# Performance work log

Measured on AMD Instinct MI355X. Metric: run time of the kernel, lower is better.

Reference implementation:

```python
import jax, jax.numpy as jnp
import numpy as np

B, S, N, D = 2, 2048, 16, 64


def setup_inputs() -> dict:
    key = jax.random.key(0)
    kq, kk, kv = jax.random.split(key, 3)
    query = jax.random.normal(kq, (B, S, N, D), dtype=jnp.float32)
    key_t = jax.random.normal(kk, (B, S, N, D), dtype=jnp.float32)
    value = jax.random.normal(kv, (B, S, N, D), dtype=jnp.float32)
    mask = jnp.ones((B, 1, S, S), dtype=jnp.int32)
    return {"query": query, "key": key_t, "value": value, "mask": mask}


def reference(query, key, value, mask):
    d_k = query.shape[-1]
    # [b, n, q, k] attention scores
    scores = jnp.einsum('bqnd,bknd->bnqk', query, key) / jnp.sqrt(jnp.float32(d_k))
    scores = jnp.where(mask == 0, -jnp.inf, scores)
    # NOTE: faithful to the source, softmax is over dim=1 (the HEAD axis),
    # not the key axis. Dropout prob is 0.0 -> identity.
    attn_weights = jax.nn.softmax(scores, axis=1)
    out = jnp.einsum('bnqk,bknd->bnqd', attn_weights, value)
    return out
```

## Files before the change

### kernel.cpp

```cpp
#include <hip/hip_runtime.h>
#include <hip/hip_bf16.h>


#define B_ 2
#define S_ 2048
#define N_ 16
#define D_ 64
#define TQ 32
#define TK 32
#define NT 64

typedef __bf16 bf16x4 __attribute__((ext_vector_type(4)));
typedef __bf16 bf16x8 __attribute__((ext_vector_type(8)));
typedef float  f32x16 __attribute__((ext_vector_type(16)));
typedef unsigned int uint32x4 __attribute__((ext_vector_type(4)));

#define QSCALE 0.18033688011112042f

static __device__ __forceinline__ unsigned int cvt_pk_bf16(float a, float b) {
    unsigned int r;
    asm("v_cvt_pk_bf16_f32 %0, %1, %2" : "=v"(r) : "v"(a), "v"(b));
    return r;
}
static __device__ __forceinline__ void permlane_swap(unsigned int& a, unsigned int& b) {
    asm("v_permlane32_swap_b32 %0, %1" : "+v"(a), "+v"(b));
}

__global__ __launch_bounds__(256) void cvt_qk_pack_kernel(
    const float* __restrict__ Qf, const float* __restrict__ Kf,
    __bf16* __restrict__ QP, __bf16* __restrict__ KP)
{
    const int z = blockIdx.z;
    const float* src = (z < B_) ? Qf : Kf;
    __bf16*      dst = (z < B_) ? QP : KP;
    const float scale = (z < B_) ? QSCALE : 1.0f;
    const int b  = (z < B_) ? z : z - B_;
    const int n  = blockIdx.y;
    const int st = blockIdx.x;
    const int t  = threadIdx.x;
    const int ks   = t >> 6;
    const int lane = t & 63;
    const int lo   = lane & 31;
    const int hi   = lane >> 5;

    const float* p = &src[(((size_t)b * S_ + st * 32 + lo) * N_ + n) * D_ + ks * 16 + hi * 8];
    const float4 a0 = *(const float4*)p;
    const float4 a1 = *(const float4*)(p + 4);
    bf16x8 o;
    o[0] = (__bf16)(a0.x * scale); o[1] = (__bf16)(a0.y * scale);
    o[2] = (__bf16)(a0.z * scale); o[3] = (__bf16)(a0.w * scale);
    o[4] = (__bf16)(a1.x * scale); o[5] = (__bf16)(a1.y * scale);
    o[6] = (__bf16)(a1.z * scale); o[7] = (__bf16)(a1.w * scale);
    *(bf16x8*)&dst[(((size_t)b * N_ + n) * NT + st) * 2048 + (size_t)t * 8] = o;
}

__global__ __launch_bounds__(256) void cvt_v_pack_kernel(
    const float* __restrict__ V, __bf16* __restrict__ VP)
{
    __shared__ __bf16 tile[64][68];
    const int s0 = blockIdx.x * 64;
    const int n  = blockIdx.y;
    const int b  = blockIdx.z;
    const int t  = threadIdx.x;

    {
        const int d4 = (t & 15) * 4;
        const int sr = t >> 4;
        #pragma unroll
        for (int r = 0; r < 4; ++r) {
            const int s = sr + r * 16;
            const float4 v = *(const float4*)&V[(((size_t)b * S_ + s0 + s) * N_ + n) * D_ + d4];
            tile[s][d4 + 0] = (__bf16)v.x;
            tile[s][d4 + 1] = (__bf16)v.y;
            tile[s][d4 + 2] = (__bf16)v.z;
            tile[s][d4 + 3] = (__bf16)v.w;
        }
    }
    __syncthreads();
    {
        const int kstep = t >> 7;
        const int dt    = (t >> 6) & 1;
        const int lane  = t & 63;
        const int lo    = lane & 31;
        const int hi    = lane >> 5;
        #pragma unroll
        for (int kt_sub = 0; kt_sub < 2; ++kt_sub) {
            bf16x8 o;
            #pragma unroll
            for (int j = 0; j < 8; ++j)
                o[j] = tile[kt_sub * 32 + kstep * 16 + hi * 8 + j][dt * 32 + lo];
            const size_t kt = (size_t)(blockIdx.x * 2 + kt_sub);
            *(bf16x8*)&VP[(((size_t)b * N_ + n) * NT + kt) * 2048 + (size_t)t * 8] = o;
        }
    }
}

__global__ __launch_bounds__(256, 3) void pass1_z_kernel(
    const __bf16* __restrict__ QP, const __bf16* __restrict__ KP,
    const int* __restrict__ M, float* __restrict__ Zrt)
{
    const int tid  = threadIdx.x;
    const int wv   = tid >> 6;
    const int lane = tid & 63;
    const int lo   = lane & 31;
    const int hi   = lane >> 5;

    const int ktA = (blockIdx.x * 4 + wv) * 2;
    const int qt  = blockIdx.y;
    const int b   = blockIdx.z;
    const int k0A = ktA * TK;
    const int q0  = qt * TQ;

    const __bf16* Qp = QP + ((size_t)b * N_ * NT + qt) * 2048 + (size_t)lane * 8;
    const __bf16* Kp = KP + ((size_t)b * N_ * NT + ktA) * 2048 + (size_t)lane * 8;

    f32x16 zA = {}, zB = {};
    #pragma unroll 2
    for (int h = 0; h < N_; ++h) {
        const __bf16* Qh = Qp + (size_t)h * NT * 2048;
        const __bf16* Kh = Kp + (size_t)h * NT * 2048;
        bf16x8 qf[4], ka[4], kb[4];
        #pragma unroll
        for (int ks = 0; ks < 4; ++ks) {
            qf[ks] = *(const bf16x8*)(Qh + ks * 512);
            ka[ks] = *(const bf16x8*)(Kh + ks * 512);
            kb[ks] = *(const bf16x8*)(Kh + 2048 + ks * 512);
        }
        f32x16 sA = {}, sB = {};
        #pragma unroll
        for (int ks = 0; ks < 4; ++ks)
            sA = __builtin_amdgcn_mfma_f32_32x32x16_bf16(ka[ks], qf[ks], sA, 0, 0, 0);
        #pragma unroll
        for (int ks = 0; ks < 4; ++ks)
            sB = __builtin_amdgcn_mfma_f32_32x32x16_bf16(kb[ks], qf[ks], sB, 0, 0, 0);
        #pragma unroll
        for (int r = 0; r < 16; ++r) {
            zA[r] += __builtin_amdgcn_exp2f(sA[r]);
            zB[r] += __builtin_amdgcn_exp2f(sB[r]);
        }
    }

    const size_t mb = (size_t)b * S_ * S_;
    int ok = 1;
    #pragma unroll
    for (int r = 0; r < 16; ++r) {
        const int2 mm = *(const int2*)&M[mb + (size_t)(q0 + 2 * r + hi) * S_ + k0A + 2 * lo];
        ok &= (mm.x != 0) & (mm.y != 0);
    }

    float vA[16], vB[16];
    #pragma unroll
    for (int r = 0; r < 16; ++r) {
        vA[r] = __builtin_amdgcn_rcpf(zA[r]);
        vB[r] = __builtin_amdgcn_rcpf(zB[r]);
    }

    if (!__all(ok)) {
        #pragma unroll
        for (int r = 0; r < 16; ++r) {
            const int kap = (r & 3) + 8 * (r >> 2) + 4 * hi;
            const size_t rowb = mb + (size_t)(q0 + lo) * S_ + k0A;
            if (M[rowb + kap] == 0)      vA[r] = __builtin_nanf("");
            if (M[rowb + 32 + kap] == 0) vB[r] = __builtin_nanf("");
        }
    }

    float* ZA = Zrt + (((size_t)b * NT + ktA) * NT + qt) * 1024 + (size_t)lane * 4;
    float* ZB = ZA + (size_t)NT * 1024;
    #pragma unroll
    for (int c = 0; c < 4; ++c) {
        *(float4*)(ZA + c * 256) = make_float4(vA[4*c], vA[4*c+1], vA[4*c+2], vA[4*c+3]);
        *(float4*)(ZB + c * 256) = make_float4(vB[4*c], vB[4*c+1], vB[4*c+2], vB[4*c+3]);
    }
}

__global__ __launch_bounds__(256, 4) void pass2_av_kernel(
    const __bf16* __restrict__ QP, const __bf16* __restrict__ KP,
    const __bf16* __restrict__ VP, const float* __restrict__ Zrt,
    float* __restrict__ O)
{
    __shared__ __align__(16) float obuf[4][16 * D_];

    const int tid  = threadIdx.x;
    const int wv   = tid >> 6;
    const int lane = tid & 63;
    const int lo   = lane & 31;
    const int hi   = lane >> 5;

    const int qt = blockIdx.x;
    const int n  = blockIdx.y;
    const int b  = blockIdx.z;
    const int q0 = qt * TQ;

    const __bf16* Qh = QP + (((size_t)b * N_ + n) * NT + qt) * 2048 + (size_t)lane * 8;
    const __bf16* Kh = KP + (((size_t)b * N_ + n) * NT) * 2048 + (size_t)lane * 8;
    const __bf16* Vh = VP + (((size_t)b * N_ + n) * NT) * 2048 + (size_t)lane * 8;
    const float*  Zh = Zrt + (size_t)b * NT * NT * 1024 + (size_t)lane * 4;

    bf16x8 qf[4];
    #pragma unroll
    for (int ks = 0; ks < 4; ++ks)
        qf[ks] = *(const bf16x8*)(Qh + ks * 512);

    f32x16 o0 = {};
    f32x16 o1 = {};

    #pragma unroll 2
    for (int t = 0; t < 16; ++t) {
        const int kt = wv * 16 + t;
        const __bf16* Kt = Kh + (size_t)kt * 2048;
        const __bf16* Vt = Vh + (size_t)kt * 2048;
        const float*  Zt = Zh + ((size_t)kt * NT + qt) * 1024;

        float4 z0 = *(const float4*)(Zt);
        float4 z1 = *(const float4*)(Zt + 256);
        float4 z2 = *(const float4*)(Zt + 512);
        float4 z3 = *(const float4*)(Zt + 768);
        float zr[16] = { z0.x, z0.y, z0.z, z0.w,  z1.x, z1.y, z1.z, z1.w,
                         z2.x, z2.y, z2.z, z2.w,  z3.x, z3.y, z3.z, z3.w };

        bf16x8 vf[2][2];
        #pragma unroll
        for (int kstep = 0; kstep < 2; ++kstep)
            #pragma unroll
            for (int dt = 0; dt < 2; ++dt)
                vf[kstep][dt] = *(const bf16x8*)(Vt + (kstep * 2 + dt) * 512);

        f32x16 s = {};
        #pragma unroll
        for (int ks = 0; ks < 4; ++ks) {
            bf16x8 kf = *(const bf16x8*)(Kt + ks * 512);
            s = __builtin_amdgcn_mfma_f32_32x32x16_bf16(kf, qf[ks], s, 0, 0, 0);
        }

        float w[16];
        #pragma unroll
        for (int r = 0; r < 16; ++r) w[r] = __builtin_amdgcn_exp2f(s[r]) * zr[r];

        #pragma unroll
        for (int kstep = 0; kstep < 2; ++kstep) {
            const int e = kstep * 8;
            unsigned int d0 = cvt_pk_bf16(w[e + 0], w[e + 1]);
            unsigned int d1 = cvt_pk_bf16(w[e + 2], w[e + 3]);
            unsigned int d2 = cvt_pk_bf16(w[e + 4], w[e + 5]);
            unsigned int d3 = cvt_pk_bf16(w[e + 6], w[e + 7]);
            permlane_swap(d0, d2);
            permlane_swap(d1, d3);
            uint32x4 u; u[0] = d0; u[1] = d1; u[2] = d2; u[3] = d3;
            const bf16x8 pa = __builtin_bit_cast(bf16x8, u);
            o0 = __builtin_amdgcn_mfma_f32_32x32x16_bf16(pa, vf[kstep][0], o0, 0, 0, 0);
            o1 = __builtin_amdgcn_mfma_f32_32x32x16_bf16(pa, vf[kstep][1], o1, 0, 0, 0);
        }
    }

    #pragma unroll
    for (int half = 0; half < 2; ++half) {
        if (half) __syncthreads();
        #pragma unroll
        for (int r8 = 0; r8 < 8; ++r8) {
            const int r  = half * 8 + r8;
            const int lr = (r8 & 3) + 8 * (r8 >> 2) + 4 * hi;
            obuf[wv][lr * D_ + lo]      = o0[r];
            obuf[wv][lr * D_ + 32 + lo] = o1[r];
        }
        __syncthreads();
        const int e0 = tid * 4;
        float a0 = 0.f, a1 = 0.f, a2 = 0.f, a3 = 0.f;
        #pragma unroll
        for (int w = 0; w < 4; ++w) {
            const float4 x = *(const float4*)&obuf[w][e0];
            a0 += x.x; a1 += x.y; a2 += x.z; a3 += x.w;
        }
        const int q = half * 16 + (e0 >> 6);
        const int d = e0 & 63;
        *(float4*)&O[(((size_t)b * N_ + n) * S_ + q0 + q) * (size_t)D_ + d]
            = make_float4(a0, a1, a2, a3);
    }
}

__global__ __launch_bounds__(1024) void sdpa_headsm_kernel(
    const float* __restrict__ Q, const float* __restrict__ K,
    const float* __restrict__ V, const int* __restrict__ M,
    float* __restrict__ O)
{
    __shared__ __align__(16) __bf16 pbuf[N_][TQ][40];

    const int tid  = threadIdx.x;
    const int n    = tid >> 6;
    const int lane = tid & 63;
    const int lo   = lane & 31;
    const int hi   = lane >> 5;

    const int q0 = blockIdx.x * TQ;
    const int b  = blockIdx.y;
    const int kz = blockIdx.z;
    const int FITERS = S_ / TK / 4;

    bf16x8 qf[4];
    {
        const float* qrow = Q + (((size_t)b * S_ + (size_t)(q0 + lo)) * N_ + n) * D_;
        #pragma unroll
        for (int ks = 0; ks < 4; ++ks) {
            const float* p = qrow + ks * 16 + hi * 8;
            float4 a0 = *(const float4*)(p);
            float4 a1 = *(const float4*)(p + 4);
            bf16x8 f;
            f[0] = (__bf16)a0.x; f[1] = (__bf16)a0.y;
            f[2] = (__bf16)a0.z; f[3] = (__bf16)a0.w;
            f[4] = (__bf16)a1.x; f[5] = (__bf16)a1.y;
            f[6] = (__bf16)a1.z; f[7] = (__bf16)a1.w;
            qf[ks] = f;
        }
    }

    f32x16 o0 = {};
    f32x16 o1 = {};

    for (int it = 0; it < FITERS; ++it) {
        const int k0 = (kz * FITERS + it) * TK;

        f32x16 s = {};
        #pragma unroll
        for (int ks = 0; ks < 4; ++ks) {
            const float* krow = K + (((size_t)b * S_ + (size_t)(k0 + lo)) * N_ + n) * D_
                                  + ks * 16 + hi * 8;
            float4 a0 = *(const float4*)(krow);
            float4 a1 = *(const float4*)(krow + 4);
            bf16x8 f;
            f[0] = (__bf16)a0.x; f[1] = (__bf16)a0.y;
            f[2] = (__bf16)a0.z; f[3] = (__bf16)a0.w;
            f[4] = (__bf16)a1.x; f[5] = (__bf16)a1.y;
            f[6] = (__bf16)a1.z; f[7] = (__bf16)a1.w;
            s = __builtin_amdgcn_mfma_f32_32x32x16_bf16(qf[ks], f, s, 0, 0, 0);
        }

        bf16x8 vf[2][2];
        #pragma unroll
        for (int kstep = 0; kstep < 2; ++kstep) {
            #pragma unroll
            for (int dt = 0; dt < 2; ++dt) {
                bf16x8 f;
                #pragma unroll
                for (int j = 0; j < 8; ++j) {
                    const int key = k0 + kstep * 16 + hi * 8 + j;
                    f[j] = (__bf16)V[(((size_t)b * S_ + key) * N_ + n) * D_ + dt * 32 + lo];
                }
                vf[kstep][dt] = f;
            }
        }

        #pragma unroll
        for (int r = 0; r < 16; ++r) {
            const int row = (r & 3) + 8 * (r >> 2) + 4 * hi;
            pbuf[n][row][lo] = (__bf16)__builtin_amdgcn_exp2f(s[r] * QSCALE);
        }

        __syncthreads();

        {
            const int tq = tid >> 5;
            const int tk = tid & 31;
            const int m = M[(size_t)b * S_ * S_ + (size_t)(q0 + tq) * S_ + (k0 + tk)];
            float pv[16];
            float sum = 0.f;
            #pragma unroll
            for (int j = 0; j < 16; ++j) { pv[j] = (float)pbuf[j][tq][tk]; sum += pv[j]; }
            const float rd = m ? (1.0f / sum) : __builtin_nanf("");
            #pragma unroll
            for (int j = 0; j < 16; ++j) pbuf[j][tq][tk] = (__bf16)(pv[j] * rd);
        }

        __syncthreads();

        #pragma unroll
        for (int kstep = 0; kstep < 2; ++kstep) {
            bf16x8 wf = *(const bf16x8*)&pbuf[n][lo][kstep * 16 + hi * 8];
            o0 = __builtin_amdgcn_mfma_f32_32x32x16_bf16(wf, vf[kstep][0], o0, 0, 0, 0);
            o1 = __builtin_amdgcn_mfma_f32_32x32x16_bf16(wf, vf[kstep][1], o1, 0, 0, 0);
        }

        __syncthreads();
    }

    #pragma unroll
    for (int r = 0; r < 16; ++r) {
        const int row = (r & 3) + 8 * (r >> 2) + 4 * hi;
        const size_t base = (((size_t)b * N_ + n) * S_ + (q0 + row)) * (size_t)D_;
        atomicAdd(&O[base + lo],      o0[r]);
        atomicAdd(&O[base + 32 + lo], o1[r]);
    }
}

extern "C" void kernel_launch(void* const* d_in, const int* in_sizes, int n_in,
                              void* d_out, int out_size, void* d_ws, size_t ws_size,
                              hipStream_t stream) {
    const float* Q = (const float*)d_in[0];
    const float* K = (const float*)d_in[1];
    const float* V = (const float*)d_in[2];
    const int*   M = (const int*)d_in[3];
    float* O = (float*)d_out;

    const size_t per  = (size_t)B_ * N_ * NT * 2048;
    const size_t zcnt = (size_t)B_ * NT * NT * 1024;
    const size_t need = 3 * per * sizeof(__bf16) + zcnt * sizeof(float);

    if (ws_size >= need) {
        __bf16* QP = (__bf16*)d_ws;
        __bf16* KP = QP + per;
        __bf16* VP = KP + per;
        float*  Zrt = (float*)(VP + per);
        cvt_qk_pack_kernel<<<dim3(NT, N_, B_ * 2), dim3(256), 0, stream>>>(Q, K, QP, KP);
        cvt_v_pack_kernel<<<dim3(S_ / 64, N_, B_), dim3(256), 0, stream>>>(V, VP);
        pass1_z_kernel<<<dim3(NT / 8, NT, B_), dim3(256), 0, stream>>>(QP, KP, M, Zrt);
        pass2_av_kernel<<<dim3(NT, N_, B_), dim3(256), 0, stream>>>(QP, KP, VP, Zrt, O);
    } else {
        hipMemsetAsync(d_out, 0, (size_t)out_size * sizeof(float), stream);
        sdpa_headsm_kernel<<<dim3(S_ / TQ, B_, 4), dim3(1024), 0, stream>>>(Q, K, V, M, O);
    }
}
```

Baseline: 220.4 us.

## Process two query tiles per wave and store head-softmax reciprocals as bf16

Both passes now handle two 32-row query tiles per block, so each loaded K/V fragment is reused for two tiles and the grid shrinks by half. The per-(q,k) reciprocal normalizer buffer is stored as bf16 instead of fp32, halving its write and read traffic between the two passes. The mask check now reads int4 rows to cover the larger tile, and occupancy hints drop to 2 blocks per CU. In exchange, register pressure goes up, there are fewer blocks to fill the GPU, and the normalizer loses precision, which adds error to the output.

Result: slower. 239.0 us (+8.4%).

```diff
diff --git a/kernel.cpp b/kernel.cpp
--- a/kernel.cpp
+++ b/kernel.cpp
@@ -95,9 +95,9 @@
     }
 }
 
-__global__ __launch_bounds__(256, 3) void pass1_z_kernel(
+__global__ __launch_bounds__(256, 2) void pass1_z_kernel(
     const __bf16* __restrict__ QP, const __bf16* __restrict__ KP,
-    const int* __restrict__ M, float* __restrict__ Zrt)
+    const int* __restrict__ M, __bf16* __restrict__ Zrb)
 {
     const int tid  = threadIdx.x;
     const int wv   = tid >> 6;
@@ -106,80 +106,103 @@
     const int hi   = lane >> 5;
 
     const int ktA = (blockIdx.x * 4 + wv) * 2;
-    const int qt  = blockIdx.y;
+    const int qt0 = blockIdx.y * 2;
     const int b   = blockIdx.z;
     const int k0A = ktA * TK;
-    const int q0  = qt * TQ;
-
-    const __bf16* Qp = QP + ((size_t)b * N_ * NT + qt) * 2048 + (size_t)lane * 8;
+    const int q0  = qt0 * TQ;
+
+    const __bf16* Qp = QP + ((size_t)b * N_ * NT + qt0) * 2048 + (size_t)lane * 8;
     const __bf16* Kp = KP + ((size_t)b * N_ * NT + ktA) * 2048 + (size_t)lane * 8;
 
-    f32x16 zA = {}, zB = {};
-    #pragma unroll 2
+    f32x16 zAA = {}, zAB = {}, zBA = {}, zBB = {};
     for (int h = 0; h < N_; ++h) {
         const __bf16* Qh = Qp + (size_t)h * NT * 2048;
         const __bf16* Kh = Kp + (size_t)h * NT * 2048;
-        bf16x8 qf[4], ka[4], kb[4];
+        bf16x8 q0f[4], q1f[4], ka[4], kb[4];
         #pragma unroll
         for (int ks = 0; ks < 4; ++ks) {
-            qf[ks] = *(const bf16x8*)(Qh + ks * 512);
-            ka[ks] = *(const bf16x8*)(Kh + ks * 512);
-            kb[ks] = *(const bf16x8*)(Kh + 2048 + ks * 512);
-        }
-        f32x16 sA = {}, sB = {};
-        #pragma unroll
-        for (int ks = 0; ks < 4; ++ks)
-            sA = __builtin_amdgcn_mfma_f32_32x32x16_bf16(ka[ks], qf[ks], sA, 0, 0, 0);
-        #pragma unroll
-        for (int ks = 0; ks < 4; ++ks)
-            sB = __builtin_amdgcn_mfma_f32_32x32x16_bf16(kb[ks], qf[ks], sB, 0, 0, 0);
-        #pragma unroll
-        for (int r = 0; r < 16; ++r) {
-            zA[r] += __builtin_amdgcn_exp2f(sA[r]);
-            zB[r] += __builtin_amdgcn_exp2f(sB[r]);
-        }
+            q0f[ks] = *(const bf16x8*)(Qh + ks * 512);
+            q1f[ks] = *(const bf16x8*)(Qh + 2048 + ks * 512);
+            ka[ks]  = *(const bf16x8*)(Kh + ks * 512);
+            kb[ks]  = *(const bf16x8*)(Kh + 2048 + ks * 512);
+        }
+        f32x16 s;
+        s = (f32x16){};
+        #pragma unroll
+        for (int ks = 0; ks < 4; ++ks) s = __builtin_amdgcn_mfma_f32_32x32x16_bf16(ka[ks], q0f[ks], s, 0, 0, 0);
+        #pragma unroll
+        for (int r = 0; r < 16; ++r) zAA[r] += __builtin_amdgcn_exp2f(s[r]);
+        s = (f32x16){};
+        #pragma unroll
+        for (int ks = 0; ks < 4; ++ks) s = __builtin_amdgcn_mfma_f32_32x32x16_bf16(ka[ks], q1f[ks], s, 0, 0, 0);
+        #pragma unroll
+        for (int r = 0; r < 16; ++r) zAB[r] += __builtin_amdgcn_exp2f(s[r]);
+        s = (f32x16){};
+        #pragma unroll
+        for (int ks = 0; ks < 4; ++ks) s = __builtin_amdgcn_mfma_f32_32x32x16_bf16(kb[ks], q0f[ks], s, 0, 0, 0);
+        #pragma unroll
+        for (int r = 0; r < 16; ++r) zBA[r] += __builtin_amdgcn_exp2f(s[r]);
+        s = (f32x16){};
+        #pragma unroll
+        for (int ks = 0; ks < 4; ++ks) s = __builtin_amdgcn_mfma_f32_32x32x16_bf16(kb[ks], q1f[ks], s, 0, 0, 0);
+        #pragma unroll
+        for (int r = 0; r < 16; ++r) zBB[r] += __builtin_amdgcn_exp2f(s[r]);
     }
 
     const size_t mb = (size_t)b * S_ * S_;
     int ok = 1;
     #pragma unroll
     for (int r = 0; r < 16; ++r) {
-        const int2 mm = *(const int2*)&M[mb + (size_t)(q0 + 2 * r + hi) * S_ + k0A + 2 * lo];
-        ok &= (mm.x != 0) & (mm.y != 0);
-    }
-
-    float vA[16], vB[16];
+        const int4 mm = *(const int4*)&M[mb + (size_t)(q0 + 4 * r + (lane >> 4)) * S_
+                                         + k0A + (lane & 15) * 4];
+        ok &= (mm.x != 0) & (mm.y != 0) & (mm.z != 0) & (mm.w != 0);
+    }
+
+    float vAA[16], vAB[16], vBA[16], vBB[16];
     #pragma unroll
     for (int r = 0; r < 16; ++r) {
-        vA[r] = __builtin_amdgcn_rcpf(zA[r]);
-        vB[r] = __builtin_amdgcn_rcpf(zB[r]);
+        vAA[r] = __builtin_amdgcn_rcpf(zAA[r]);
+        vAB[r] = __builtin_amdgcn_rcpf(zAB[r]);
+        vBA[r] = __builtin_amdgcn_rcpf(zBA[r]);
+        vBB[r] = __builtin_amdgcn_rcpf(zBB[r]);
     }
 
     if (!__all(ok)) {
         #pragma unroll
         for (int r = 0; r < 16; ++r) {
             const int kap = (r & 3) + 8 * (r >> 2) + 4 * hi;
-            const size_t rowb = mb + (size_t)(q0 + lo) * S_ + k0A;
-            if (M[rowb + kap] == 0)      vA[r] = __builtin_nanf("");
-            if (M[rowb + 32 + kap] == 0) vB[r] = __builtin_nanf("");
-        }
-    }
-
-    float* ZA = Zrt + (((size_t)b * NT + ktA) * NT + qt) * 1024 + (size_t)lane * 4;
-    float* ZB = ZA + (size_t)NT * 1024;
-    #pragma unroll
-    for (int c = 0; c < 4; ++c) {
-        *(float4*)(ZA + c * 256) = make_float4(vA[4*c], vA[4*c+1], vA[4*c+2], vA[4*c+3]);
-        *(float4*)(ZB + c * 256) = make_float4(vB[4*c], vB[4*c+1], vB[4*c+2], vB[4*c+3]);
-    }
-}
-
-__global__ __launch_bounds__(256, 4) void pass2_av_kernel(
+            const size_t rowA = mb + (size_t)(q0 + lo) * S_;
+            const size_t rowB = mb + (size_t)(q0 + 32 + lo) * S_;
+            if (M[rowA + k0A + kap] == 0)      vAA[r] = __builtin_nanf("");
+            if (M[rowB + k0A + kap] == 0)      vAB[r] = __builtin_nanf("");
+            if (M[rowA + k0A + 32 + kap] == 0) vBA[r] = __builtin_nanf("");
+            if (M[rowB + k0A + 32 + kap] == 0) vBB[r] = __builtin_nanf("");
+        }
+    }
+
+    auto store_tile = [&](const float (&v)[16], int kt_, int qt_) {
+        __bf16* Zt = Zrb + (((size_t)b * NT + kt_) * NT + qt_) * 1024 + (size_t)lane * 8;
+        #pragma unroll
+        for (int g = 0; g < 2; ++g) {
+            uint32x4 u;
+            #pragma unroll
+            for (int i = 0; i < 4; ++i)
+                u[i] = cvt_pk_bf16(v[g * 8 + 2 * i], v[g * 8 + 2 * i + 1]);
+            *(bf16x8*)(Zt + g * 512) = __builtin_bit_cast(bf16x8, u);
+        }
+    };
+    store_tile(vAA, ktA,     qt0);
+    store_tile(vAB, ktA,     qt0 + 1);
+    store_tile(vBA, ktA + 1, qt0);
+    store_tile(vBB, ktA + 1, qt0 + 1);
+}
+
+__global__ __launch_bounds__(256, 2) void pass2_av_kernel(
     const __bf16* __restrict__ QP, const __bf16* __restrict__ KP,
-    const __bf16* __restrict__ VP, const float* __restrict__ Zrt,
+    const __bf16* __restrict__ VP, const __bf16* __restrict__ Zrb,
     float* __restrict__ O)
 {
-    __shared__ __align__(16) float obuf[4][16 * D_];
+    __shared__ __align__(16) float obuf[4][TQ * D_];
 
     const int tid  = threadIdx.x;
     const int wv   = tid >> 6;
@@ -187,38 +210,39 @@
     const int lo   = lane & 31;
     const int hi   = lane >> 5;
 
-    const int qt = blockIdx.x;
-    const int n  = blockIdx.y;
-    const int b  = blockIdx.z;
-    const int q0 = qt * TQ;
-
-    const __bf16* Qh = QP + (((size_t)b * N_ + n) * NT + qt) * 2048 + (size_t)lane * 8;
+    const int n   = blockIdx.x;
+    const int qt0 = blockIdx.y * 2;
+    const int b   = blockIdx.z;
+
+    const __bf16* Qh = QP + (((size_t)b * N_ + n) * NT + qt0) * 2048 + (size_t)lane * 8;
     const __bf16* Kh = KP + (((size_t)b * N_ + n) * NT) * 2048 + (size_t)lane * 8;
     const __bf16* Vh = VP + (((size_t)b * N_ + n) * NT) * 2048 + (size_t)lane * 8;
-    const float*  Zh = Zrt + (size_t)b * NT * NT * 1024 + (size_t)lane * 4;
-
-    bf16x8 qf[4];
+    const __bf16* Zb = Zrb + (size_t)b * NT * NT * 1024 + (size_t)lane * 8;
+
+    bf16x8 qf0[4], qf1[4];
     #pragma unroll
-    for (int ks = 0; ks < 4; ++ks)
-        qf[ks] = *(const bf16x8*)(Qh + ks * 512);
-
-    f32x16 o0 = {};
-    f32x16 o1 = {};
-
-    #pragma unroll 2
+    for (int ks = 0; ks < 4; ++ks) {
+        qf0[ks] = *(const bf16x8*)(Qh + ks * 512);
+        qf1[ks] = *(const bf16x8*)(Qh + 2048 + ks * 512);
+    }
+
+    f32x16 o00 = {}, o01 = {};
+    f32x16 o10 = {}, o11 = {};
+
     for (int t = 0; t < 16; ++t) {
         const int kt = wv * 16 + t;
         const __bf16* Kt = Kh + (size_t)kt * 2048;
         const __bf16* Vt = Vh + (size_t)kt * 2048;
-        const float*  Zt = Zh + ((size_t)kt * NT + qt) * 1024;
-
-        float4 z0 = *(const float4*)(Zt);
-        float4 z1 = *(const float4*)(Zt + 256);
-        float4 z2 = *(const float4*)(Zt + 512);
-        float4 z3 = *(const float4*)(Zt + 768);
-        float zr[16] = { z0.x, z0.y, z0.z, z0.w,  z1.x, z1.y, z1.z, z1.w,
-                         z2.x, z2.y, z2.z, z2.w,  z3.x, z3.y, z3.z, z3.w };
-
+        const __bf16* Zt = Zb + ((size_t)kt * NT + qt0) * 1024;
+
+        const bf16x8 z0a = *(const bf16x8*)(Zt);
+        const bf16x8 z0b = *(const bf16x8*)(Zt + 512);
+        const bf16x8 z1a = *(const bf16x8*)(Zt + 1024);
+        const bf16x8 z1b = *(const bf16x8*)(Zt + 1536);
+
+        bf16x8 kf[4];
+        #pragma unroll
+        for (int ks = 0; ks < 4; ++ks) kf[ks] = *(const bf16x8*)(Kt + ks * 512);
         bf16x8 vf[2][2];
         #pragma unroll
         for (int kstep = 0; kstep < 2; ++kstep)
@@ -226,56 +250,84 @@
             for (int dt = 0; dt < 2; ++dt)
                 vf[kstep][dt] = *(const bf16x8*)(Vt + (kstep * 2 + dt) * 512);
 
-        f32x16 s = {};
+        f32x16 s0 = {}, s1 = {};
         #pragma unroll
         for (int ks = 0; ks < 4; ++ks) {
-            bf16x8 kf = *(const bf16x8*)(Kt + ks * 512);
-            s = __builtin_amdgcn_mfma_f32_32x32x16_bf16(kf, qf[ks], s, 0, 0, 0);
-        }
-
-        float w[16];
-        #pragma unroll
-        for (int r = 0; r < 16; ++r) w[r] = __builtin_amdgcn_exp2f(s[r]) * zr[r];
-
-        #pragma unroll
-        for (int kstep = 0; kstep < 2; ++kstep) {
-            const int e = kstep * 8;
-            unsigned int d0 = cvt_pk_bf16(w[e + 0], w[e + 1]);
-            unsigned int d1 = cvt_pk_bf16(w[e + 2], w[e + 3]);
-            unsigned int d2 = cvt_pk_bf16(w[e + 4], w[e + 5]);
-            unsigned int d3 = cvt_pk_bf16(w[e + 6], w[e + 7]);
-            permlane_swap(d0, d2);
-            permlane_swap(d1, d3);
-            uint32x4 u; u[0] = d0; u[1] = d1; u[2] = d2; u[3] = d3;
-            const bf16x8 pa = __builtin_bit_cast(bf16x8, u);
-            o0 = __builtin_amdgcn_mfma_f32_32x32x16_bf16(pa, vf[kstep][0], o0, 0, 0, 0);
-            o1 = __builtin_amdgcn_mfma_f32_32x32x16_bf16(pa, vf[kstep][1], o1, 0, 0, 0);
-        }
-    }
-
-    #pragma unroll
-    for (int half = 0; half < 2; ++half) {
-        if (half) __syncthreads();
-        #pragma unroll
-        for (int r8 = 0; r8 < 8; ++r8) {
-            const int r  = half * 8 + r8;
-            const int lr = (r8 & 3) + 8 * (r8 >> 2) + 4 * hi;
-            obuf[wv][lr * D_ + lo]      = o0[r];
-            obuf[wv][lr * D_ + 32 + lo] = o1[r];
+            s0 = __builtin_amdgcn_mfma_f32_32x32x16_bf16(kf[ks], qf0[ks], s0, 0, 0, 0);
+            s1 = __builtin_amdgcn_mfma_f32_32x32x16_bf16(kf[ks], qf1[ks], s1, 0, 0, 0);
+        }
+
+        {
+            float w[16];
+            #pragma unroll
+            for (int r = 0; r < 8; ++r)  w[r] = __builtin_amdgcn_exp2f(s0[r]) * (float)z0a[r];
+            #pragma unroll
+            for (int r = 8; r < 16; ++r) w[r] = __builtin_amdgcn_exp2f(s0[r]) * (float)z0b[r - 8];
+            #pragma unroll
+            for (int kstep = 0; kstep < 2; ++kstep) {
+                const int e = kstep * 8;
+                unsigned int d0 = cvt_pk_bf16(w[e + 0], w[e + 1]);
+                unsigned int d1 = cvt_pk_bf16(w[e + 2], w[e + 3]);
+                unsigned int d2 = cvt_pk_bf16(w[e + 4], w[e + 5]);
+                unsigned int d3 = cvt_pk_bf16(w[e + 6], w[e + 7]);
+                permlane_swap(d0, d2);
+                permlane_swap(d1, d3);
+                uint32x4 u; u[0] = d0; u[1] = d1; u[2] = d2; u[3] = d3;
+                const bf16x8 pa = __builtin_bit_cast(bf16x8, u);
+                o00 = __builtin_amdgcn_mfma_f32_32x32x16_bf16(pa, vf[kstep][0], o00, 0, 0, 0);
+                o01 = __builtin_amdgcn_mfma_f32_32x32x16_bf16(pa, vf[kstep][1], o01, 0, 0, 0);
+            }
+        }
+        {
+            float w[16];
+            #pragma unroll
+            for (int r = 0; r < 8; ++r)  w[r] = __builtin_amdgcn_exp2f(s1[r]) * (float)z1a[r];
+            #pragma unroll
+            for (int r = 8; r < 16; ++r) w[r] = __builtin_amdgcn_exp2f(s1[r]) * (float)z1b[r - 8];
+            #pragma unroll
+            for (int kstep = 0; kstep < 2; ++kstep) {
+                const int e = kstep * 8;
+                unsigned int d0 = cvt_pk_bf16(w[e + 0], w[e + 1]);
+                unsigned int d1 = cvt_pk_bf16(w[e + 2], w[e + 3]);
+                unsigned int d2 = cvt_pk_bf16(w[e + 4], w[e + 5]);
+                unsigned int d3 = cvt_pk_bf16(w[e + 6], w[e + 7]);
+                permlane_swap(d0, d2);
+                permlane_swap(d1, d3);
+                uint32x4 u; u[0] = d0; u[1] = d1; u[2] = d2; u[3] = d3;
+                const bf16x8 pa = __builtin_bit_cast(bf16x8, u);
+                o10 = __builtin_amdgcn_mfma_f32_32x32x16_bf16(pa, vf[kstep][0], o10, 0, 0, 0);
+                o11 = __builtin_amdgcn_mfma_f32_32x32x16_bf16(pa, vf[kstep][1], o11, 0, 0, 0);
+            }
+        }
+    }
+
+    auto combine_store = [&](const f32x16& a0, const f32x16& a1, int qt_) {
+        #pragma unroll
+        for (int r = 0; r < 16; ++r) {
+            const int row = (r & 3) + 8 * (r >> 2) + 4 * hi;
+            obuf[wv][row * D_ + lo]      = a0[r];
+            obuf[wv][row * D_ + 32 + lo] = a1[r];
         }
         __syncthreads();
-        const int e0 = tid * 4;
-        float a0 = 0.f, a1 = 0.f, a2 = 0.f, a3 = 0.f;
+        const int e0 = tid * 8;
+        float b0 = 0.f, b1 = 0.f, b2 = 0.f, b3 = 0.f;
+        float b4 = 0.f, b5 = 0.f, b6 = 0.f, b7 = 0.f;
         #pragma unroll
         for (int w = 0; w < 4; ++w) {
             const float4 x = *(const float4*)&obuf[w][e0];
-            a0 += x.x; a1 += x.y; a2 += x.z; a3 += x.w;
-        }
-        const int q = half * 16 + (e0 >> 6);
+            const float4 y = *(const float4*)&obuf[w][e0 + 4];
+            b0 += x.x; b1 += x.y; b2 += x.z; b3 += x.w;
+            b4 += y.x; b5 += y.y; b6 += y.z; b7 += y.w;
+        }
+        const int q = e0 >> 6;
         const int d = e0 & 63;
-        *(float4*)&O[(((size_t)b * N_ + n) * S_ + q0 + q) * (size_t)D_ + d]
-            = make_float4(a0, a1, a2, a3);
-    }
+        float* dst = &O[(((size_t)b * N_ + n) * S_ + qt_ * TQ + q) * (size_t)D_ + d];
+        *(float4*)dst       = make_float4(b0, b1, b2, b3);
+        *(float4*)(dst + 4) = make_float4(b4, b5, b6, b7);
+    };
+    combine_store(o00, o01, qt0);
+    __syncthreads();
+    combine_store(o10, o11, qt0 + 1);
 }
 
 __global__ __launch_bounds__(1024) void sdpa_headsm_kernel(
@@ -402,17 +454,17 @@
 
     const size_t per  = (size_t)B_ * N_ * NT * 2048;
     const size_t zcnt = (size_t)B_ * NT * NT * 1024;
-    const size_t need = 3 * per * sizeof(__bf16) + zcnt * sizeof(float);
+    const size_t need = (3 * per + zcnt) * sizeof(__bf16);
 
     if (ws_size >= need) {
         __bf16* QP = (__bf16*)d_ws;
         __bf16* KP = QP + per;
         __bf16* VP = KP + per;
-        float*  Zrt = (float*)(VP + per);
+        __bf16* Zrb = VP + per;
         cvt_qk_pack_kernel<<<dim3(NT, N_, B_ * 2), dim3(256), 0, stream>>>(Q, K, QP, KP);
         cvt_v_pack_kernel<<<dim3(S_ / 64, N_, B_), dim3(256), 0, stream>>>(V, VP);
-        pass1_z_kernel<<<dim3(NT / 8, NT, B_), dim3(256), 0, stream>>>(QP, KP, M, Zrt);
-        pass2_av_kernel<<<dim3(NT, N_, B_), dim3(256), 0, stream>>>(QP, KP, VP, Zrt, O);
+        pass1_z_kernel<<<dim3(NT / 8, NT / 2, B_), dim3(256), 0, stream>>>(QP, KP, M, Zrb);
+        pass2_av_kernel<<<dim3(N_, NT / 2, B_), dim3(256), 0, stream>>>(QP, KP, VP, Zrb, O);
     } else {
         hipMemsetAsync(d_out, 0, (size_t)out_size * sizeof(float), stream);
         sdpa_headsm_kernel<<<dim3(S_ / TQ, B_, 4), dim3(1024), 0, stream>>>(Q, K, V, M, O);
```
